# Performance work log

Hardware: AMD Instinct MI355X
Metric: run time of the kernel (lower is better)

Reference implementation:

```python
import jax, jax.numpy as jnp
import numpy as np
from jax import lax

BN_EPS = 1e-5

def _conv1x1(x, w):
    # x: [B,C,H,W], w: [O,C] -> [B,O,H,W]
    return jnp.einsum('bchw,oc->bohw', x, w)

def _box7(u):
    # 7x7 all-ones box filter, padding 3 (same as F.conv2d(u, ones(1,1,7,7), padding=3))
    k = jnp.ones((1, 1, 7, 7), u.dtype)
    return lax.conv_general_dilated(u, k, (1, 1), ((3, 3), (3, 3)),
                                    dimension_numbers=('NCHW', 'OIHW', 'NCHW'))

def setup_inputs() -> dict:
    key = jax.random.key(0)
    ks = jax.random.split(key, 8)
    B, C, H, W = 8, 256, 128, 128
    x = jax.random.normal(ks[0], (B, C, H, W), jnp.float32)
    W_proj = jax.random.normal(ks[1], (C, C), jnp.float32) * (1.0 / np.sqrt(C))
    gamma = jnp.ones((C,), jnp.float32)
    beta = jnp.zeros((C,), jnp.float32)
    W_conv = jax.random.normal(ks[2], (C, C), jnp.float32) * (1.0 / np.sqrt(C))
    b_conv = jnp.zeros((C,), jnp.float32)
    W_mean = jax.random.normal(ks[3], (1, C), jnp.float32) * 0.05
    W_std = jax.random.normal(ks[4], (1, C), jnp.float32) * 0.05
    eps1 = jax.random.normal(ks[5], (B, 1, H, W), jnp.float32)
    eps50 = jax.random.normal(ks[6], (B, 50, H, W), jnp.float32)
    rand_u = jax.random.uniform(ks[7], (B, 1, H, W), jnp.float32)
    return {'x': x, 'W_proj': W_proj, 'gamma': gamma, 'beta': beta,
            'W_conv': W_conv, 'b_conv': b_conv, 'W_mean': W_mean, 'W_std': W_std,
            'eps1': eps1, 'eps50': eps50, 'rand_u': rand_u}

def reference(x, W_proj, gamma, beta, W_conv, b_conv, W_mean, W_std, eps1, eps50, rand_u):
    # input_proj: 1x1 conv (no bias) -> BatchNorm (training: batch stats) -> ReLU (dropout = identity)
    h = _conv1x1(x, W_proj)
    mu = jnp.mean(h, axis=(0, 2, 3), keepdims=True)
    var = jnp.var(h, axis=(0, 2, 3), keepdims=True)
    h = (h - mu) * lax.rsqrt(var + BN_EPS)
    h = h * gamma[None, :, None, None] + beta[None, :, None, None]
    h = jax.nn.relu(h)

    residual = _conv1x1(h, W_conv) + b_conv[None, :, None, None]  # [B,C,H,W]
    mean = _conv1x1(h, W_mean)    # [B,1,H,W]
    logvar = _conv1x1(h, W_std)   # [B,1,H,W]
    std = jnp.exp(0.5 * logvar)

    prob_x = eps1 * std + mean                      # reparameterize, iter=1
    prob_out = jax.nn.sigmoid(eps50 * std + mean)   # reparameterize, iter=50 (broadcast over 50 samples)

    # torch .var(dim=1) default is unbiased -> ddof=1; .detach() -> stop_gradient
    u = jnp.var(prob_out, axis=1, keepdims=True, ddof=1)
    u = lax.stop_gradient(u)

    # training: three sequential 7x7 box filters
    u = _box7(_box7(_box7(u)))
    u = (u - u.min()) / (u.max() - u.min())

    residual = residual * (1.0 - u)
    mask = (u < rand_u).astype(residual.dtype)
    residual = residual * mask
    return residual, prob_x
```

## Files before the change

### kernel.cpp

```cpp
#include <hip/hip_runtime.h>

#define HW   16384
#define CC   256
#define OT   32
#define NT   512
#define KB   8

typedef float          f32x4  __attribute__((ext_vector_type(4)));
typedef short          bf16x8 __attribute__((ext_vector_type(8)));
typedef unsigned short u16x8  __attribute__((ext_vector_type(8)));

__device__ inline unsigned short f2bf(float x) {
    unsigned u = __float_as_uint(x);
    u += 0x7FFFu + ((u >> 16) & 1u);
    return (unsigned short)(u >> 16);
}
__device__ inline float bf2f(unsigned short h) {
    return __uint_as_float(((unsigned)h) << 16);
}


__global__ __launch_bounds__(256)
void gu_xsplit(const float* __restrict__ x, unsigned short* __restrict__ xhiT,
               unsigned short* __restrict__ xloT)
{
    __shared__ float T[64][257];
    const int t = threadIdx.x;
    const int l = t & 63, w = t >> 6;
    const int n0 = blockIdx.x * 64;
    const int b  = n0 >> 14;
    const int hw0 = n0 & (HW - 1);
    const float* xb = x + (size_t)b * CC * HW + hw0;

    #pragma unroll 4
    for (int it = 0; it < 32; ++it) {
        int cl = it * 2 + (l >> 5);
        int c  = w * 64 + cl;
        int nn = (l & 31) * 2;
        float2 v = *(const float2*)(xb + (size_t)c * HW + nn);
        T[nn][c]     = v.x;
        T[nn + 1][c] = v.y;
    }
    __syncthreads();

    #pragma unroll
    for (int it = 0; it < 8; ++it) {
        int i = it * 256 + t;
        int row = i >> 5, ch = i & 31;
        unsigned short vh[8], vl[8];
        #pragma unroll
        for (int e = 0; e < 8; ++e) {
            float v = T[row][ch * 8 + e];
            unsigned short hh = f2bf(v);
            vh[e] = hh;
            vl[e] = f2bf(v - bf2f(hh));
        }
        size_t dst = (size_t)(n0 + row) * CC + ch * 8;
        *(u16x8*)&xhiT[dst] = *(u16x8*)vh;
        *(u16x8*)&xloT[dst] = *(u16x8*)vl;
    }
}

__global__ __launch_bounds__(256)
void gu_wsplit2(const float* __restrict__ Wp, const float* __restrict__ Wc,
                unsigned short* __restrict__ Wphi, unsigned short* __restrict__ Wplo,
                unsigned short* __restrict__ Wchi, unsigned short* __restrict__ Wclo)
{
    int i = blockIdx.x * 256 + threadIdx.x;
    if (i < 65536) {
        float w = Wp[i];
        unsigned short hh = f2bf(w);
        Wphi[i] = hh;
        Wplo[i] = f2bf(w - bf2f(hh));
    } else {
        int j = i - 65536;
        float w = Wc[j];
        unsigned short hh = f2bf(w);
        Wchi[j] = hh;
        Wclo[j] = f2bf(w - bf2f(hh));
    }
}

__global__ __launch_bounds__(256)
void gu_gemm1m(const unsigned short* __restrict__ xhiT, const unsigned short* __restrict__ xloT,
               const unsigned short* __restrict__ Wphi, const unsigned short* __restrict__ Wplo,
               float* __restrict__ h, float* __restrict__ psum, float* __restrict__ psumsq)
{
    __shared__ unsigned short Wh[128 * 64], Wl[128 * 64];
    __shared__ unsigned short Xh[128 * 64], Xl[128 * 64];
    __shared__ float sredS[128], sredQ[128];

    const int t   = threadIdx.x;
    const int l   = t & 63;
    const int wid = t >> 6;
    const int wo  = (wid & 1) * 64;
    const int wn  = (wid >> 1) * 64;
    const int n0  = blockIdx.x * 128;
    const int o0  = blockIdx.y * 128;
    const int b   = n0 >> 14;
    const int hw0 = n0 & (HW - 1);

    f32x4 acc[4][4];
    #pragma unroll
    for (int m = 0; m < 4; ++m)
        #pragma unroll
        for (int nn = 0; nn < 4; ++nn) acc[m][nn] = (f32x4){0.f, 0.f, 0.f, 0.f};

    for (int kt = 0; kt < 4; ++kt) {
        const int c0 = kt * 64;
        #pragma unroll
        for (int q = 0; q < 4; ++q) {
            int chunk = t + 256 * q;
            int row = chunk >> 3, ch = chunk & 7;
            int dst = row * 64 + ((ch ^ (row & 7)) << 3);
            size_t wsrc = (size_t)(o0 + row) * CC + c0 + (ch << 3);
            size_t xsrc = (size_t)(n0 + row) * CC + c0 + (ch << 3);
            *(u16x8*)&Wh[dst] = *(const u16x8*)&Wphi[wsrc];
            *(u16x8*)&Wl[dst] = *(const u16x8*)&Wplo[wsrc];
            *(u16x8*)&Xh[dst] = *(const u16x8*)&xhiT[xsrc];
            *(u16x8*)&Xl[dst] = *(const u16x8*)&xloT[xsrc];
        }
        __syncthreads();
        #pragma unroll
        for (int ks = 0; ks < 2; ++ks) {
            bf16x8 ah[4], al[4], bh[4], bl[4];
            #pragma unroll
            for (int m = 0; m < 4; ++m) {
                int row = wo + m * 16 + (l & 15);
                int idx = row * 64 + ((((ks << 2) + (l >> 4)) ^ (row & 7)) << 3);
                ah[m] = *(const bf16x8*)&Wh[idx];
                al[m] = *(const bf16x8*)&Wl[idx];
            }
            #pragma unroll
            for (int nn = 0; nn < 4; ++nn) {
                int row = wn + nn * 16 + (l & 15);
                int idx = row * 64 + ((((ks << 2) + (l >> 4)) ^ (row & 7)) << 3);
                bh[nn] = *(const bf16x8*)&Xh[idx];
                bl[nn] = *(const bf16x8*)&Xl[idx];
            }
            #pragma unroll
            for (int m = 0; m < 4; ++m)
                #pragma unroll
                for (int nn = 0; nn < 4; ++nn) {
                    acc[m][nn] = __builtin_amdgcn_mfma_f32_16x16x32_bf16(ah[m], bh[nn], acc[m][nn], 0, 0, 0);
                    acc[m][nn] = __builtin_amdgcn_mfma_f32_16x16x32_bf16(ah[m], bl[nn], acc[m][nn], 0, 0, 0);
                    acc[m][nn] = __builtin_amdgcn_mfma_f32_16x16x32_bf16(al[m], bh[nn], acc[m][nn], 0, 0, 0);
                }
        }
        __syncthreads();
    }

    float sst[4][4], qst[4][4];
    #pragma unroll
    for (int m = 0; m < 4; ++m) {
        int ob = wo + m * 16 + ((l >> 4) << 2);
        #pragma unroll
        for (int j = 0; j < 4; ++j) {
            float s = 0.f, qq = 0.f;
            #pragma unroll
            for (int nn = 0; nn < 4; ++nn) {
                float v = acc[m][nn][j];
                h[((size_t)(b * CC + o0 + ob + j)) * HW + hw0 + wn + nn * 16 + (l & 15)] = v;
                s += v; qq = fmaf(v, v, qq);
            }
            #pragma unroll
            for (int off = 1; off < 16; off <<= 1) {
                s  += __shfl_xor(s, off);
                qq += __shfl_xor(qq, off);
            }
            sst[m][j] = s; qst[m][j] = qq;
            if (wn == 0 && (l & 15) == 0) { sredS[ob + j] = s; sredQ[ob + j] = qq; }
        }
    }
    __syncthreads();
    if (wn == 64 && (l & 15) == 0) {
        #pragma unroll
        for (int m = 0; m < 4; ++m) {
            int ob = wo + m * 16 + ((l >> 4) << 2);
            #pragma unroll
            for (int j = 0; j < 4; ++j) {
                atomicAdd(&psum[o0 + ob + j],   sst[m][j] + sredS[ob + j]);
                atomicAdd(&psumsq[o0 + ob + j], qst[m][j] + sredQ[ob + j]);
            }
        }
    }
}

__global__ void gu_bnfin(const float* __restrict__ psum, const float* __restrict__ psumsq,
                         const float* __restrict__ gamma, const float* __restrict__ beta,
                         float* __restrict__ avec, float* __restrict__ dvec)
{
    int c = threadIdx.x;
    const float invN = 1.f / 131072.f;
    float mu  = psum[c] * invN;
    float var = psumsq[c] * invN - mu * mu;
    float a   = gamma[c] * rsqrtf(var + 1e-5f);
    avec[c] = a;
    dvec[c] = beta[c] - mu * a;
}

__global__ __launch_bounds__(256)
void gu_projsplit(const float* __restrict__ h, const float* __restrict__ Wm,
                  const float* __restrict__ Wsd, const float* __restrict__ avec,
                  const float* __restrict__ dvec, const float* __restrict__ eps1,
                  const float* __restrict__ eps50, float* __restrict__ prob_x,
                  float* __restrict__ u0, unsigned short* __restrict__ rT)
{
    __shared__ float s_a[CC], s_d[CC], s_m[CC], s_v[CC];
    int t = threadIdx.x;
    s_a[t] = avec[t]; s_d[t] = dvec[t]; s_m[t] = Wm[t]; s_v[t] = Wsd[t];
    __syncthreads();

    int p  = blockIdx.x * 256 + t;
    int b  = p >> 14;
    int hw = p & (HW - 1);
    const float* hb = h + (size_t)b * CC * HW + hw;
    unsigned short* pr = rT + (size_t)p * CC;

    float mp = 0.f, lp = 0.f;
    for (int c0 = 0; c0 < CC; c0 += 8) {
        unsigned short v8[8];
        #pragma unroll
        for (int e = 0; e < 8; ++e) {
            float v = hb[(size_t)(c0 + e) * HW];
            float r = fmaxf(fmaf(s_a[c0 + e], v, s_d[c0 + e]), 0.f);
            mp = fmaf(s_m[c0 + e], r, mp);
            lp = fmaf(s_v[c0 + e], r, lp);
            v8[e] = f2bf(r);
        }
        *(u16x8*)&pr[c0] = *(u16x8*)v8;
    }
    float std = expf(0.5f * lp);
    prob_x[p] = fmaf(eps1[p], std, mp);

    const float* e5 = eps50 + (size_t)b * 50 * HW + hw;
    double s = 0.0, q = 0.0;
    #pragma unroll 5
    for (int k = 0; k < 50; ++k) {
        float z = fmaf(e5[(size_t)k * HW], std, mp);
        float pr2 = 1.f / (1.f + expf(-z));
        s += (double)pr2;
        q += (double)pr2 * (double)pr2;
    }
    u0[p] = (float)((q - s * s * (1.0 / 50.0)) * (1.0 / 49.0));
}

__global__ __launch_bounds__(1024)
void gu_box(const float* __restrict__ u0, float* __restrict__ u3,
            unsigned* __restrict__ mnb, unsigned* __restrict__ mxb)
{
    __shared__ float A[HW];
    int b = blockIdx.x, t = threadIdx.x;
    const float* src = u0 + (size_t)b * HW;
    for (int i = t; i < HW; i += 1024) A[i] = src[i];
    __syncthreads();

    float tmp[16];
    for (int pass = 0; pass < 3; ++pass) {
        #pragma unroll
        for (int ii = 0; ii < 16; ++ii) {
            int i = t + ii * 1024;
            int r = i >> 7, c = i & 127;
            float s = 0.f;
            #pragma unroll
            for (int d = -3; d <= 3; ++d) {
                int cc = c + d;
                if (cc >= 0 && cc < 128) s += A[(r << 7) + cc];
            }
            tmp[ii] = s;
        }
        __syncthreads();
        #pragma unroll
        for (int ii = 0; ii < 16; ++ii) A[t + ii * 1024] = tmp[ii];
        __syncthreads();
        #pragma unroll
        for (int ii = 0; ii < 16; ++ii) {
            int i = t + ii * 1024;
            int r = i >> 7, c = i & 127;
            float s = 0.f;
            #pragma unroll
            for (int d = -3; d <= 3; ++d) {
                int rr = r + d;
                if (rr >= 0 && rr < 128) s += A[(rr << 7) + c];
            }
            tmp[ii] = s;
        }
        __syncthreads();
        #pragma unroll
        for (int ii = 0; ii < 16; ++ii) A[t + ii * 1024] = tmp[ii];
        __syncthreads();
    }

    float mn = 3.4e38f, mx = 0.f;
    for (int i = t; i < HW; i += 1024) {
        float v = A[i];
        u3[(size_t)b * HW + i] = v;
        mn = fminf(mn, v); mx = fmaxf(mx, v);
    }
    #pragma unroll
    for (int off = 1; off < 64; off <<= 1) {
        mn = fminf(mn, __shfl_xor(mn, off));
        mx = fmaxf(mx, __shfl_xor(mx, off));
    }
    if ((t & 63) == 0) {
        atomicMin(mnb, __float_as_uint(mn));
        atomicMax(mxb, __float_as_uint(mx));
    }
}

__global__ __launch_bounds__(256)
void gu_gemm2m(const unsigned short* __restrict__ Wchi, const unsigned short* __restrict__ Wclo,
               const unsigned short* __restrict__ rT, const float* __restrict__ bconv,
               const float* __restrict__ u3, const unsigned* __restrict__ mnb,
               const unsigned* __restrict__ mxb, const float* __restrict__ ru,
               float* __restrict__ outr)
{
    __shared__ unsigned short Wh[128 * 64], Wl[128 * 64], Rh[128 * 64];

    const int t   = threadIdx.x;
    const int l   = t & 63;
    const int wid = t >> 6;
    const int wo  = (wid & 1) * 64;
    const int wn  = (wid >> 1) * 64;
    const int n0  = blockIdx.x * 128;
    const int o0  = blockIdx.y * 128;
    const int b   = n0 >> 14;
    const int hw0 = n0 & (HW - 1);

    f32x4 acc[4][4];
    #pragma unroll
    for (int m = 0; m < 4; ++m)
        #pragma unroll
        for (int nn = 0; nn < 4; ++nn) acc[m][nn] = (f32x4){0.f, 0.f, 0.f, 0.f};

    for (int kt = 0; kt < 4; ++kt) {
        const int c0 = kt * 64;
        #pragma unroll
        for (int q = 0; q < 4; ++q) {
            int chunk = t + 256 * q;
            int row = chunk >> 3, ch = chunk & 7;
            int dst = row * 64 + ((ch ^ (row & 7)) << 3);
            size_t wsrc = (size_t)(o0 + row) * CC + c0 + (ch << 3);
            size_t rsrc = (size_t)(n0 + row) * CC + c0 + (ch << 3);
            *(u16x8*)&Wh[dst] = *(const u16x8*)&Wchi[wsrc];
            *(u16x8*)&Wl[dst] = *(const u16x8*)&Wclo[wsrc];
            *(u16x8*)&Rh[dst] = *(const u16x8*)&rT[rsrc];
        }
        __syncthreads();
        #pragma unroll
        for (int ks = 0; ks < 2; ++ks) {
            bf16x8 ah[4], al[4], bh[4];
            #pragma unroll
            for (int m = 0; m < 4; ++m) {
                int row = wo + m * 16 + (l & 15);
                int idx = row * 64 + ((((ks << 2) + (l >> 4)) ^ (row & 7)) << 3);
                ah[m] = *(const bf16x8*)&Wh[idx];
                al[m] = *(const bf16x8*)&Wl[idx];
            }
            #pragma unroll
            for (int nn = 0; nn < 4; ++nn) {
                int row = wn + nn * 16 + (l & 15);
                int idx = row * 64 + ((((ks << 2) + (l >> 4)) ^ (row & 7)) << 3);
                bh[nn] = *(const bf16x8*)&Rh[idx];
            }
            #pragma unroll
            for (int m = 0; m < 4; ++m)
                #pragma unroll
                for (int nn = 0; nn < 4; ++nn) {
                    acc[m][nn] = __builtin_amdgcn_mfma_f32_16x16x32_bf16(ah[m], bh[nn], acc[m][nn], 0, 0, 0);
                    acc[m][nn] = __builtin_amdgcn_mfma_f32_16x16x32_bf16(al[m], bh[nn], acc[m][nn], 0, 0, 0);
                }
        }
        __syncthreads();
    }

    float mn = __uint_as_float(*mnb);
    float mx = __uint_as_float(*mxb);
    float den = mx - mn;
    float scv[4];
    #pragma unroll
    for (int nn = 0; nn < 4; ++nn) {
        int hw = hw0 + wn + nn * 16 + (l & 15);
        float un = (u3[(size_t)b * HW + hw] - mn) / den;
        scv[nn] = (un < ru[(size_t)b * HW + hw]) ? (1.f - un) : 0.f;
    }
    #pragma unroll
    for (int m = 0; m < 4; ++m) {
        int obase = o0 + wo + m * 16 + ((l >> 4) << 2);
        #pragma unroll
        for (int j = 0; j < 4; ++j) {
            float bc = bconv[obase + j];
            #pragma unroll
            for (int nn = 0; nn < 4; ++nn) {
                int hw = hw0 + wn + nn * 16 + (l & 15);
                outr[((size_t)(b * CC + obase + j)) * HW + hw] = (acc[m][nn][j] + bc) * scv[nn];
            }
        }
    }
}

__global__ __launch_bounds__(256)
void gu_gemm1(const float* __restrict__ x, const float* __restrict__ Wp,
              float* __restrict__ h, float* __restrict__ psum,
              float* __restrict__ psumsq)
{
    __shared__ float xs[2][KB][NT];
    const int t  = threadIdx.x;
    const int tx = t & 63, ty = t >> 6;
    const int tyu = __builtin_amdgcn_readfirstlane(ty);
    const int o0 = blockIdx.y * OT;
    const int n0 = blockIdx.x * NT;
    const int b  = n0 >> 14;
    const int hw0 = n0 & (HW - 1);
    const float* xb = x + ((size_t)b * CC) * HW + hw0;
    const float* Wb = Wp + (size_t)(o0 + tyu * 8) * CC;

    float4 pf[4];
    #pragma unroll
    for (int q = 0; q < 4; ++q) {
        int f = t + 256 * q; int k = f >> 7; int co = (f & 127) << 2;
        pf[q] = *(const float4*)(xb + (size_t)k * HW + co);
    }
    float acc[8][8];
    #pragma unroll
    for (int i = 0; i < 8; ++i)
        #pragma unroll
        for (int j = 0; j < 8; ++j) acc[i][j] = 0.f;

    int wb = 0;
    for (int c0 = 0; c0 < CC; c0 += KB) {
        #pragma unroll
        for (int q = 0; q < 4; ++q) {
            int f = t + 256 * q; int k = f >> 7; int co = (f & 127) << 2;
            *(float4*)&xs[wb][k][co] = pf[q];
        }
        if (c0 + KB < CC) {
            #pragma unroll
            for (int q = 0; q < 4; ++q) {
                int f = t + 256 * q; int k = f >> 7; int co = (f & 127) << 2;
                pf[q] = *(const float4*)(xb + (size_t)(c0 + KB + k) * HW + co);
            }
        }
        __syncthreads();
        #pragma unroll
        for (int half = 0; half < 2; ++half) {
            float4 wq[8];
            #pragma unroll
            for (int i = 0; i < 8; ++i)
                wq[i] = *(const float4*)(Wb + (size_t)i * CC + c0 + half * 4);
            #pragma unroll
            for (int kk = 0; kk < 4; ++kk) {
                int k = half * 4 + kk;
                float4 xa = *(const float4*)&xs[wb][k][tx * 4];
                float4 xc = *(const float4*)&xs[wb][k][256 + tx * 4];
                #pragma unroll
                for (int i = 0; i < 8; ++i) {
                    float w = ((const float*)&wq[i])[kk];
                    acc[i][0] = fmaf(w, xa.x, acc[i][0]);
                    acc[i][1] = fmaf(w, xa.y, acc[i][1]);
                    acc[i][2] = fmaf(w, xa.z, acc[i][2]);
                    acc[i][3] = fmaf(w, xa.w, acc[i][3]);
                    acc[i][4] = fmaf(w, xc.x, acc[i][4]);
                    acc[i][5] = fmaf(w, xc.y, acc[i][5]);
                    acc[i][6] = fmaf(w, xc.z, acc[i][6]);
                    acc[i][7] = fmaf(w, xc.w, acc[i][7]);
                }
            }
        }
        __syncthreads();
        wb ^= 1;
    }
    #pragma unroll
    for (int i = 0; i < 8; ++i) {
        float* hp = h + ((size_t)(b * CC + o0 + ty * 8 + i)) * HW + hw0 + tx * 4;
        *(float4*)hp         = make_float4(acc[i][0], acc[i][1], acc[i][2], acc[i][3]);
        *(float4*)(hp + 256) = make_float4(acc[i][4], acc[i][5], acc[i][6], acc[i][7]);
    }
    #pragma unroll
    for (int i = 0; i < 8; ++i) {
        float s = 0.f, q = 0.f;
        #pragma unroll
        for (int j = 0; j < 8; ++j) { s += acc[i][j]; q = fmaf(acc[i][j], acc[i][j], q); }
        #pragma unroll
        for (int off = 1; off < 64; off <<= 1) {
            s += __shfl_xor(s, off);
            q += __shfl_xor(q, off);
        }
        if (tx == 0) {
            atomicAdd(&psum[o0 + ty * 8 + i], s);
            atomicAdd(&psumsq[o0 + ty * 8 + i], q);
        }
    }
}

__global__ __launch_bounds__(256)
void gu_proj(const float* __restrict__ h, const float* __restrict__ Wm,
             const float* __restrict__ Wsd, const float* __restrict__ avec,
             const float* __restrict__ dvec, const float* __restrict__ eps1,
             const float* __restrict__ eps50, float* __restrict__ prob_x,
             float* __restrict__ u0)
{
    __shared__ float s_a[CC], s_d[CC], s_m[CC], s_v[CC];
    int t = threadIdx.x;
    s_a[t] = avec[t]; s_d[t] = dvec[t]; s_m[t] = Wm[t]; s_v[t] = Wsd[t];
    __syncthreads();
    int p  = blockIdx.x * 256 + t;
    int b  = p >> 14;
    int hw = p & (HW - 1);
    const float* hb = h + (size_t)b * CC * HW + hw;
    float mp = 0.f, lp = 0.f;
    #pragma unroll 8
    for (int c = 0; c < CC; ++c) {
        float v = hb[(size_t)c * HW];
        float r = fmaxf(fmaf(s_a[c], v, s_d[c]), 0.f);
        mp = fmaf(s_m[c], r, mp);
        lp = fmaf(s_v[c], r, lp);
    }
    float std = expf(0.5f * lp);
    prob_x[p] = fmaf(eps1[p], std, mp);
    const float* e5 = eps50 + (size_t)b * 50 * HW + hw;
    double s = 0.0, q = 0.0;
    #pragma unroll 5
    for (int k = 0; k < 50; ++k) {
        float z = fmaf(e5[(size_t)k * HW], std, mp);
        float pr = 1.f / (1.f + expf(-z));
        s += (double)pr;
        q += (double)pr * (double)pr;
    }
    u0[p] = (float)((q - s * s * (1.0 / 50.0)) * (1.0 / 49.0));
}

__global__ __launch_bounds__(256)
void gu_gemm2(const float* __restrict__ h, const float* __restrict__ Wc,
              const float* __restrict__ bconv, const float* __restrict__ avec,
              const float* __restrict__ dvec, const float* __restrict__ u3,
              const unsigned* __restrict__ mnb, const unsigned* __restrict__ mxb,
              const float* __restrict__ ru, float* __restrict__ outr)
{
    __shared__ float xs[2][KB][NT];
    __shared__ float sa[CC], sd[CC];
    const int t  = threadIdx.x;
    const int tx = t & 63, ty = t >> 6;
    const int tyu = __builtin_amdgcn_readfirstlane(ty);
    const int o0 = blockIdx.y * OT;
    const int n0 = blockIdx.x * NT;
    const int b  = n0 >> 14;
    const int hw0 = n0 & (HW - 1);
    const float* xb = h + ((size_t)b * CC) * HW + hw0;
    const float* Wb = Wc + (size_t)(o0 + tyu * 8) * CC;

    sa[t] = avec[t]; sd[t] = dvec[t];
    float4 pf[4];
    #pragma unroll
    for (int q = 0; q < 4; ++q) {
        int f = t + 256 * q; int k = f >> 7; int co = (f & 127) << 2;
        pf[q] = *(const float4*)(xb + (size_t)k * HW + co);
    }
    float acc[8][8];
    #pragma unroll
    for (int i = 0; i < 8; ++i)
        #pragma unroll
        for (int j = 0; j < 8; ++j) acc[i][j] = 0.f;

    __syncthreads();
    int wb = 0;
    for (int c0 = 0; c0 < CC; c0 += KB) {
        #pragma unroll
        for (int q = 0; q < 4; ++q) {
            int f = t + 256 * q; int k = f >> 7; int co = (f & 127) << 2;
            float a = sa[c0 + k], d = sd[c0 + k];
            float4 v = pf[q];
            v.x = fmaxf(fmaf(a, v.x, d), 0.f);
            v.y = fmaxf(fmaf(a, v.y, d), 0.f);
            v.z = fmaxf(fmaf(a, v.z, d), 0.f);
            v.w = fmaxf(fmaf(a, v.w, d), 0.f);
            *(float4*)&xs[wb][k][co] = v;
        }
        if (c0 + KB < CC) {
            #pragma unroll
            for (int q = 0; q < 4; ++q) {
                int f = t + 256 * q; int k = f >> 7; int co = (f & 127) << 2;
                pf[q] = *(const float4*)(xb + (size_t)(c0 + KB + k) * HW + co);
            }
        }
        __syncthreads();
        #pragma unroll
        for (int half = 0; half < 2; ++half) {
            float4 wq[8];
            #pragma unroll
            for (int i = 0; i < 8; ++i)
                wq[i] = *(const float4*)(Wb + (size_t)i * CC + c0 + half * 4);
            #pragma unroll
            for (int kk = 0; kk < 4; ++kk) {
                int k = half * 4 + kk;
                float4 xa = *(const float4*)&xs[wb][k][tx * 4];
                float4 xc = *(const float4*)&xs[wb][k][256 + tx * 4];
                #pragma unroll
                for (int i = 0; i < 8; ++i) {
                    float w = ((const float*)&wq[i])[kk];
                    acc[i][0] = fmaf(w, xa.x, acc[i][0]);
                    acc[i][1] = fmaf(w, xa.y, acc[i][1]);
                    acc[i][2] = fmaf(w, xa.z, acc[i][2]);
                    acc[i][3] = fmaf(w, xa.w, acc[i][3]);
                    acc[i][4] = fmaf(w, xc.x, acc[i][4]);
                    acc[i][5] = fmaf(w, xc.y, acc[i][5]);
                    acc[i][6] = fmaf(w, xc.z, acc[i][6]);
                    acc[i][7] = fmaf(w, xc.w, acc[i][7]);
                }
            }
        }
        __syncthreads();
        wb ^= 1;
    }
    float mn = __uint_as_float(*mnb);
    float mx = __uint_as_float(*mxb);
    float den = mx - mn;
    const float* u3b = u3 + (size_t)b * HW + hw0 + tx * 4;
    const float* rub = ru + (size_t)b * HW + hw0 + tx * 4;
    float sc[8];
    #pragma unroll
    for (int j = 0; j < 8; ++j) {
        int off = (j < 4) ? j : 256 + (j - 4);
        float un = (u3b[off] - mn) / den;
        sc[j] = (un < rub[off]) ? (1.f - un) : 0.f;
    }
    #pragma unroll
    for (int i = 0; i < 8; ++i) {
        float bc = bconv[o0 + ty * 8 + i];
        float* op = outr + ((size_t)(b * CC + o0 + ty * 8 + i)) * HW + hw0 + tx * 4;
        *(float4*)op = make_float4((acc[i][0] + bc) * sc[0], (acc[i][1] + bc) * sc[1],
                                   (acc[i][2] + bc) * sc[2], (acc[i][3] + bc) * sc[3]);
        *(float4*)(op + 256) = make_float4((acc[i][4] + bc) * sc[4], (acc[i][5] + bc) * sc[5],
                                           (acc[i][6] + bc) * sc[6], (acc[i][7] + bc) * sc[7]);
    }
}

extern "C" void kernel_launch(void* const* d_in, const int* in_sizes, int n_in,
                              void* d_out, int out_size, void* d_ws, size_t ws_size,
                              hipStream_t stream)
{
    const float* x     = (const float*)d_in[0];
    const float* Wp    = (const float*)d_in[1];
    const float* gamma = (const float*)d_in[2];
    const float* beta  = (const float*)d_in[3];
    const float* Wc    = (const float*)d_in[4];
    const float* bconv = (const float*)d_in[5];
    const float* Wm    = (const float*)d_in[6];
    const float* Wsd   = (const float*)d_in[7];
    const float* eps1  = (const float*)d_in[8];
    const float* eps50 = (const float*)d_in[9];
    const float* ru    = (const float*)d_in[10];

    float* outr = (float*)d_out;
    float* outp = outr + (size_t)33554432;

    float* ws = (float*)d_ws;
    float* h  = ws;
    const size_t S = (size_t)33554432;
    float*    psum   = ws + S;
    float*    psumsq = ws + S + 256;
    float*    avec   = ws + S + 512;
    float*    dvec   = ws + S + 768;
    unsigned* mnb    = (unsigned*)(ws + S + 1024);
    unsigned* mxb    = (unsigned*)(ws + S + 1025);
    float*    u0     = ws + S + 2048;
    float*    u3     = u0 + 131072;
    unsigned short* rT   = (unsigned short*)(ws + S + 264192);
    unsigned short* Wphi = rT + (size_t)33554432;
    unsigned short* Wplo = Wphi + 65536;
    unsigned short* Wchi = Wplo + 65536;
    unsigned short* Wclo = Wchi + 65536;

    unsigned short* xhiT = (unsigned short*)d_out;
    unsigned short* xloT = xhiT + (size_t)33554432;

    const size_t WS_NEED = (size_t)(S + 264192) * 4 + (size_t)33554432 * 2 + 4 * 65536 * 2;
    const bool use_mfma = (ws_size >= WS_NEED);

    hipMemsetAsync(psum, 0, 512 * sizeof(float), stream);
    hipMemsetAsync(mnb, 0x7f, 4, stream);
    hipMemsetAsync(mxb, 0, 4, stream);

    if (use_mfma) {
        gu_xsplit<<<2048, 256, 0, stream>>>(x, xhiT, xloT);
        gu_wsplit2<<<512, 256, 0, stream>>>(Wp, Wc, Wphi, Wplo, Wchi, Wclo);
        gu_gemm1m<<<dim3(1024, 2), 256, 0, stream>>>(xhiT, xloT, Wphi, Wplo, h, psum, psumsq);
        gu_bnfin<<<1, 256, 0, stream>>>(psum, psumsq, gamma, beta, avec, dvec);
        gu_projsplit<<<512, 256, 0, stream>>>(h, Wm, Wsd, avec, dvec, eps1, eps50, outp, u0, rT);
        gu_box<<<8, 1024, 0, stream>>>(u0, u3, mnb, mxb);
        gu_gemm2m<<<dim3(1024, 2), 256, 0, stream>>>(Wchi, Wclo, rT, bconv, u3, mnb, mxb, ru, outr);
    } else {
        gu_gemm1<<<dim3(256, 8), 256, 0, stream>>>(x, Wp, h, psum, psumsq);
        gu_bnfin<<<1, 256, 0, stream>>>(psum, psumsq, gamma, beta, avec, dvec);
        gu_proj<<<512, 256, 0, stream>>>(h, Wm, Wsd, avec, dvec, eps1, eps50, outp, u0);
        gu_box<<<8, 1024, 0, stream>>>(u0, u3, mnb, mxb);
        gu_gemm2<<<dim3(256, 8), 256, 0, stream>>>(h, Wc, bconv, avec, dvec, u3, mnb, mxb, ru, outr);
    }
}
```

Baseline: 644.2 us.

## Pre-swizzle weights into MFMA fragment order and stream activations via direct-to-LDS loads

The weight split kernel now writes the bf16 hi/lo weights in the per-lane MFMA fragment layout, so the GEMMs read A fragments straight from global memory (L2-resident) instead of staging them through shared memory. Activation tiles are loaded with global_load_lds (direct global-to-LDS) using an XOR-swizzled source address in place of register-staged copies. This cuts LDS footprint and LDS write/read traffic, which may raise occupancy. The trade-off is per-iteration global loads for weights inside the MFMA loop, which could expose latency.

```diff
diff --git a/kernel.cpp b/kernel.cpp
--- a/kernel.cpp
+++ b/kernel.cpp
@@ -17,6 +17,12 @@
 }
 __device__ inline float bf2f(unsigned short h) {
     return __uint_as_float(((unsigned)h) << 16);
+}
+
+__device__ inline void gload16(const void* g, void* s) {
+    __builtin_amdgcn_global_load_lds(
+        (const __attribute__((address_space(1))) void*)g,
+        (__attribute__((address_space(3))) void*)s, 16, 0, 0);
 }
 
 
@@ -62,31 +68,37 @@
 }
 
 __global__ __launch_bounds__(256)
-void gu_wsplit2(const float* __restrict__ Wp, const float* __restrict__ Wc,
-                unsigned short* __restrict__ Wphi, unsigned short* __restrict__ Wplo,
-                unsigned short* __restrict__ Wchi, unsigned short* __restrict__ Wclo)
-{
-    int i = blockIdx.x * 256 + threadIdx.x;
-    if (i < 65536) {
-        float w = Wp[i];
+void gu_wsplitf(const float* __restrict__ Wp, const float* __restrict__ Wc,
+                unsigned short* __restrict__ Wpfh, unsigned short* __restrict__ Wpfl,
+                unsigned short* __restrict__ Wcfh, unsigned short* __restrict__ Wcfl)
+{
+    int q = blockIdx.x * 256 + threadIdx.x;
+    const float* W       = (q < 8192) ? Wp  : Wc;
+    unsigned short* Fh   = (q < 8192) ? Wpfh : Wcfh;
+    unsigned short* Fl   = (q < 8192) ? Wpfl : Wcfl;
+    int qq  = q & 8191;
+    int ot  = qq >> 9;
+    int ks  = (qq >> 6) & 7;
+    int l   = qq & 63;
+    int row = ot * 16 + (l & 15);
+    int col = ks * 32 + (l >> 4) * 8;
+    unsigned short vh[8], vl[8];
+    #pragma unroll
+    for (int e = 0; e < 8; ++e) {
+        float w = W[row * CC + col + e];
         unsigned short hh = f2bf(w);
-        Wphi[i] = hh;
-        Wplo[i] = f2bf(w - bf2f(hh));
-    } else {
-        int j = i - 65536;
-        float w = Wc[j];
-        unsigned short hh = f2bf(w);
-        Wchi[j] = hh;
-        Wclo[j] = f2bf(w - bf2f(hh));
-    }
+        vh[e] = hh;
+        vl[e] = f2bf(w - bf2f(hh));
+    }
+    *(u16x8*)&Fh[(size_t)qq * 8] = *(u16x8*)vh;
+    *(u16x8*)&Fl[(size_t)qq * 8] = *(u16x8*)vl;
 }
 
 __global__ __launch_bounds__(256)
 void gu_gemm1m(const unsigned short* __restrict__ xhiT, const unsigned short* __restrict__ xloT,
-               const unsigned short* __restrict__ Wphi, const unsigned short* __restrict__ Wplo,
+               const unsigned short* __restrict__ Wpfh, const unsigned short* __restrict__ Wpfl,
                float* __restrict__ h, float* __restrict__ psum, float* __restrict__ psumsq)
 {
-    __shared__ unsigned short Wh[128 * 64], Wl[128 * 64];
     __shared__ unsigned short Xh[128 * 64], Xl[128 * 64];
     __shared__ float sredS[128], sredQ[128];
 
@@ -99,6 +111,10 @@
     const int o0  = blockIdx.y * 128;
     const int b   = n0 >> 14;
     const int hw0 = n0 & (HW - 1);
+    const int otb = (o0 >> 4) + ((wid & 1) << 2);
+
+    const int srow = l >> 3;
+    const int scd  = (l & 7) ^ srow;
 
     f32x4 acc[4][4];
     #pragma unroll
@@ -109,28 +125,19 @@
     for (int kt = 0; kt < 4; ++kt) {
         const int c0 = kt * 64;
         #pragma unroll
-        for (int q = 0; q < 4; ++q) {
-            int chunk = t + 256 * q;
-            int row = chunk >> 3, ch = chunk & 7;
-            int dst = row * 64 + ((ch ^ (row & 7)) << 3);
-            size_t wsrc = (size_t)(o0 + row) * CC + c0 + (ch << 3);
-            size_t xsrc = (size_t)(n0 + row) * CC + c0 + (ch << 3);
-            *(u16x8*)&Wh[dst] = *(const u16x8*)&Wphi[wsrc];
-            *(u16x8*)&Wl[dst] = *(const u16x8*)&Wplo[wsrc];
-            *(u16x8*)&Xh[dst] = *(const u16x8*)&xhiT[xsrc];
-            *(u16x8*)&Xl[dst] = *(const u16x8*)&xloT[xsrc];
+        for (int j = 0; j < 4; ++j) {
+            int rbase = (j * 4 + wid) * 8;
+            int row   = rbase + srow;
+            const unsigned short* sh = xhiT + (size_t)(n0 + row) * CC + c0 + scd * 8;
+            const unsigned short* sl = xloT + (size_t)(n0 + row) * CC + c0 + scd * 8;
+            gload16(sh, &Xh[rbase * 64]);
+            gload16(sl, &Xl[rbase * 64]);
         }
         __syncthreads();
         #pragma unroll
         for (int ks = 0; ks < 2; ++ks) {
-            bf16x8 ah[4], al[4], bh[4], bl[4];
-            #pragma unroll
-            for (int m = 0; m < 4; ++m) {
-                int row = wo + m * 16 + (l & 15);
-                int idx = row * 64 + ((((ks << 2) + (l >> 4)) ^ (row & 7)) << 3);
-                ah[m] = *(const bf16x8*)&Wh[idx];
-                al[m] = *(const bf16x8*)&Wl[idx];
-            }
+            const int ksg = kt * 2 + ks;
+            bf16x8 bh[4], bl[4];
             #pragma unroll
             for (int nn = 0; nn < 4; ++nn) {
                 int row = wn + nn * 16 + (l & 15);
@@ -139,13 +146,17 @@
                 bl[nn] = *(const bf16x8*)&Xl[idx];
             }
             #pragma unroll
-            for (int m = 0; m < 4; ++m)
+            for (int m = 0; m < 4; ++m) {
+                size_t off = ((size_t)((otb + m) * 8 + ksg) * 64 + l) * 8;
+                bf16x8 ah = *(const bf16x8*)&Wpfh[off];
+                bf16x8 al = *(const bf16x8*)&Wpfl[off];
                 #pragma unroll
                 for (int nn = 0; nn < 4; ++nn) {
-                    acc[m][nn] = __builtin_amdgcn_mfma_f32_16x16x32_bf16(ah[m], bh[nn], acc[m][nn], 0, 0, 0);
-                    acc[m][nn] = __builtin_amdgcn_mfma_f32_16x16x32_bf16(ah[m], bl[nn], acc[m][nn], 0, 0, 0);
-                    acc[m][nn] = __builtin_amdgcn_mfma_f32_16x16x32_bf16(al[m], bh[nn], acc[m][nn], 0, 0, 0);
+                    acc[m][nn] = __builtin_amdgcn_mfma_f32_16x16x32_bf16(ah, bh[nn], acc[m][nn], 0, 0, 0);
+                    acc[m][nn] = __builtin_amdgcn_mfma_f32_16x16x32_bf16(ah, bl[nn], acc[m][nn], 0, 0, 0);
+                    acc[m][nn] = __builtin_amdgcn_mfma_f32_16x16x32_bf16(al, bh[nn], acc[m][nn], 0, 0, 0);
                 }
+            }
         }
         __syncthreads();
     }
@@ -309,13 +320,13 @@
 }
 
 __global__ __launch_bounds__(256)
-void gu_gemm2m(const unsigned short* __restrict__ Wchi, const unsigned short* __restrict__ Wclo,
+void gu_gemm2m(const unsigned short* __restrict__ Wcfh, const unsigned short* __restrict__ Wcfl,
                const unsigned short* __restrict__ rT, const float* __restrict__ bconv,
                const float* __restrict__ u3, const unsigned* __restrict__ mnb,
                const unsigned* __restrict__ mxb, const float* __restrict__ ru,
                float* __restrict__ outr)
 {
-    __shared__ unsigned short Wh[128 * 64], Wl[128 * 64], Rh[128 * 64];
+    __shared__ unsigned short Rh[128 * 64];
 
     const int t   = threadIdx.x;
     const int l   = t & 63;
@@ -326,6 +337,10 @@
     const int o0  = blockIdx.y * 128;
     const int b   = n0 >> 14;
     const int hw0 = n0 & (HW - 1);
+    const int otb = (o0 >> 4) + ((wid & 1) << 2);
+
+    const int srow = l >> 3;
+    const int scd  = (l & 7) ^ srow;
 
     f32x4 acc[4][4];
     #pragma unroll
@@ -336,27 +351,17 @@
     for (int kt = 0; kt < 4; ++kt) {
         const int c0 = kt * 64;
         #pragma unroll
-        for (int q = 0; q < 4; ++q) {
-            int chunk = t + 256 * q;
-            int row = chunk >> 3, ch = chunk & 7;
-            int dst = row * 64 + ((ch ^ (row & 7)) << 3);
-            size_t wsrc = (size_t)(o0 + row) * CC + c0 + (ch << 3);
-            size_t rsrc = (size_t)(n0 + row) * CC + c0 + (ch << 3);
-            *(u16x8*)&Wh[dst] = *(const u16x8*)&Wchi[wsrc];
-            *(u16x8*)&Wl[dst] = *(const u16x8*)&Wclo[wsrc];
-            *(u16x8*)&Rh[dst] = *(const u16x8*)&rT[rsrc];
+        for (int j = 0; j < 4; ++j) {
+            int rbase = (j * 4 + wid) * 8;
+            int row   = rbase + srow;
+            const unsigned short* sr = rT + (size_t)(n0 + row) * CC + c0 + scd * 8;
+            gload16(sr, &Rh[rbase * 64]);
         }
         __syncthreads();
         #pragma unroll
         for (int ks = 0; ks < 2; ++ks) {
-            bf16x8 ah[4], al[4], bh[4];
-            #pragma unroll
-            for (int m = 0; m < 4; ++m) {
-                int row = wo + m * 16 + (l & 15);
-                int idx = row * 64 + ((((ks << 2) + (l >> 4)) ^ (row & 7)) << 3);
-                ah[m] = *(const bf16x8*)&Wh[idx];
-                al[m] = *(const bf16x8*)&Wl[idx];
-            }
+            const int ksg = kt * 2 + ks;
+            bf16x8 bh[4];
             #pragma unroll
             for (int nn = 0; nn < 4; ++nn) {
                 int row = wn + nn * 16 + (l & 15);
@@ -364,12 +369,16 @@
                 bh[nn] = *(const bf16x8*)&Rh[idx];
             }
             #pragma unroll
-            for (int m = 0; m < 4; ++m)
+            for (int m = 0; m < 4; ++m) {
+                size_t off = ((size_t)((otb + m) * 8 + ksg) * 64 + l) * 8;
+                bf16x8 ah = *(const bf16x8*)&Wcfh[off];
+                bf16x8 al = *(const bf16x8*)&Wcfl[off];
                 #pragma unroll
                 for (int nn = 0; nn < 4; ++nn) {
-                    acc[m][nn] = __builtin_amdgcn_mfma_f32_16x16x32_bf16(ah[m], bh[nn], acc[m][nn], 0, 0, 0);
-                    acc[m][nn] = __builtin_amdgcn_mfma_f32_16x16x32_bf16(al[m], bh[nn], acc[m][nn], 0, 0, 0);
+                    acc[m][nn] = __builtin_amdgcn_mfma_f32_16x16x32_bf16(ah, bh[nn], acc[m][nn], 0, 0, 0);
+                    acc[m][nn] = __builtin_amdgcn_mfma_f32_16x16x32_bf16(al, bh[nn], acc[m][nn], 0, 0, 0);
                 }
+            }
         }
         __syncthreads();
     }
@@ -666,10 +675,10 @@
     float*    u0     = ws + S + 2048;
     float*    u3     = u0 + 131072;
     unsigned short* rT   = (unsigned short*)(ws + S + 264192);
-    unsigned short* Wphi = rT + (size_t)33554432;
-    unsigned short* Wplo = Wphi + 65536;
-    unsigned short* Wchi = Wplo + 65536;
-    unsigned short* Wclo = Wchi + 65536;
+    unsigned short* Wpfh = rT + (size_t)33554432;
+    unsigned short* Wpfl = Wpfh + 65536;
+    unsigned short* Wcfh = Wpfl + 65536;
+    unsigned short* Wcfl = Wcfh + 65536;
 
     unsigned short* xhiT = (unsigned short*)d_out;
     unsigned short* xloT = xhiT + (size_t)33554432;
@@ -683,12 +692,12 @@
 
     if (use_mfma) {
         gu_xsplit<<<2048, 256, 0, stream>>>(x, xhiT, xloT);
-        gu_wsplit2<<<512, 256, 0, stream>>>(Wp, Wc, Wphi, Wplo, Wchi, Wclo);
-        gu_gemm1m<<<dim3(1024, 2), 256, 0, stream>>>(xhiT, xloT, Wphi, Wplo, h, psum, psumsq);
+        gu_wsplitf<<<64, 256, 0, stream>>>(Wp, Wc, Wpfh, Wpfl, Wcfh, Wcfl);
+        gu_gemm1m<<<dim3(1024, 2), 256, 0, stream>>>(xhiT, xloT, Wpfh, Wpfl, h, psum, psumsq);
         gu_bnfin<<<1, 256, 0, stream>>>(psum, psumsq, gamma, beta, avec, dvec);
         gu_projsplit<<<512, 256, 0, stream>>>(h, Wm, Wsd, avec, dvec, eps1, eps50, outp, u0, rT);
         gu_box<<<8, 1024, 0, stream>>>(u0, u3, mnb, mxb);
-        gu_gemm2m<<<dim3(1024, 2), 256, 0, stream>>>(Wchi, Wclo, rT, bconv, u3, mnb, mxb, ru, outr);
+        gu_gemm2m<<<dim3(1024, 2), 256, 0, stream>>>(Wcfh, Wcfl, rT, bconv, u3, mnb, mxb, ru, outr);
     } else {
         gu_gemm1<<<dim3(256, 8), 256, 0, stream>>>(x, Wp, h, psum, psumsq);
         gu_bnfin<<<1, 256, 0, stream>>>(psum, psumsq, gamma, beta, avec, dvec);
```

Result: slower. 695.8 us (+8.0%).
